# Performance work log

Hardware: AMD Instinct MI355X
Metric: run time of the kernel (lower is better)

## Reference

```python
import jax, jax.numpy as jnp
import numpy as np

N_NODES = 50000
N_EDGES = 800000
IN_FEAT = 256
OUT_FEAT = 256
NUM_RELS = 8
ALPHA = 0.5


def setup_inputs() -> dict:
    key = jax.random.key(0)
    k1, k2, k3, k4, k5, k6 = jax.random.split(key, 6)
    x = jax.random.normal(k1, (N_NODES, IN_FEAT), dtype=jnp.float32)
    edge_index = jax.random.randint(k2, (2, N_EDGES), 0, N_NODES, dtype=jnp.int64)
    edge_type = jax.random.randint(k3, (N_EDGES,), 0, NUM_RELS, dtype=jnp.int64)
    # Xavier-uniform-ish init for weights (scale per fan-in/fan-out)
    gain = float(np.sqrt(2.0))  # calculate_gain('relu')
    lim_w = gain * float(np.sqrt(6.0 / (IN_FEAT + OUT_FEAT)))
    weight = jax.random.uniform(k4, (NUM_RELS, IN_FEAT, OUT_FEAT), dtype=jnp.float32,
                                minval=-lim_w, maxval=lim_w)
    loop_weight = jax.random.uniform(k5, (IN_FEAT, OUT_FEAT), dtype=jnp.float32,
                                     minval=-lim_w, maxval=lim_w)
    h_bias = jnp.zeros((OUT_FEAT,), dtype=jnp.float32)
    return {"edge_index": edge_index, "x": x, "edge_type": edge_type,
            "weight": weight, "h_bias": h_bias, "loop_weight": loop_weight}


def reference(edge_index, x, edge_type, weight, h_bias, loop_weight):
    num_nodes = x.shape[0]
    src, dst = edge_index[0], edge_index[1]
    # Per-edge message msg_e = x[src_e] @ weight[edge_type_e].
    # Computed efficiently as num_rels dense GEMMs over all nodes, then a fused
    # (relation, src) gather — identical math, avoids (E, in, out) weight blowup.
    hx = jnp.einsum('ni,rio->rno', x, weight)          # (R, N, out)
    msg = hx[edge_type, src]                            # (E, out)
    agg = jax.ops.segment_sum(msg, dst, num_segments=num_nodes)  # (N, out)
    node_repr = agg * jnp.asarray(ALPHA, x.dtype) ** 0.5
    node_repr = node_repr + h_bias
    loop_message = x @ loop_weight                      # (N, out)
    node_repr = node_repr + loop_message * jnp.asarray(1.0 - ALPHA, x.dtype) ** 0.5
    # activation=None, dropout=0.0 (eval) -> identity
    return node_repr
```

## Files before the change

kernel.cpp:

```cpp
#include <hip/hip_runtime.h>

typedef __bf16 bf16x8 __attribute__((ext_vector_type(8)));
typedef float f32x4 __attribute__((ext_vector_type(4)));

static __device__ __forceinline__ unsigned short f2bf(float f) {
    unsigned u = __builtin_bit_cast(unsigned, f);
    u += 0x7FFFu + ((u >> 16) & 1u);
    return (unsigned short)(u >> 16);
}
static __device__ __forceinline__ float bf2f(unsigned short h) {
    return __builtin_bit_cast(float, ((unsigned)h) << 16);
}

#define GLOAD_LDS16(g, l)                                              \
    __builtin_amdgcn_global_load_lds(                                  \
        (const __attribute__((address_space(1))) unsigned int*)(g),    \
        (__attribute__((address_space(3))) unsigned int*)(l), 16, 0, 0)

__global__ __launch_bounds__(256) void rgcn_prep(const int* __restrict__ ei,
                                                 unsigned* __restrict__ cnt,
                                                 const float* __restrict__ x,
                                                 unsigned short* __restrict__ Z,
                                                 const float* __restrict__ w,
                                                 const float* __restrict__ lw,
                                                 unsigned short* __restrict__ wbT,
                                                 int E, int M, int HB, int CB) {
    const int b = blockIdx.x;
    const int t = threadIdx.x;
    if (b < HB) {
        int e = b * 256 + t;
        if (e < E) atomicAdd(&cnt[ei[E + e]], 1u);
    } else if (b < HB + CB) {
        int wv = ((b - HB) * 256 + t) >> 6;
        int lane = t & 63;
        if (wv < M) {
            float4 v = *(const float4*)(x + (size_t)wv * 256 + lane * 4);
            ushort4 o;
            o.x = f2bf(v.x); o.y = f2bf(v.y); o.z = f2bf(v.z); o.w = f2bf(v.w);
            *(ushort4*)(Z + (size_t)wv * 2304 + 2048 + lane * 4) = o;
        }
    } else {
        int bb = b - HB - CB;
        int kc = (bb % 9) * 256 + t;
        int n  = bb / 9;
        if (kc < 2304) {
            float v;
            if (kc < 2048) {
                int r = kc >> 8, k = kc & 255;
                v = w[((size_t)r * 256 + k) * 256 + n];
            } else {
                v = lw[(size_t)(kc - 2048) * 256 + n];
            }
            wbT[(size_t)n * 2304 + kc] = f2bf(v * 0.70710678118654752f);
        }
    }
}

__global__ __launch_bounds__(1024) void rgcn_scan_all(const unsigned* __restrict__ cnt,
                                                      unsigned* __restrict__ off,
                                                      unsigned* __restrict__ cur,
                                                      unsigned* __restrict__ done,
                                                      unsigned* __restrict__ bsum,
                                                      int n, int nb) {
    __shared__ unsigned wsum[16];
    __shared__ unsigned bpre_s;
    const int t = threadIdx.x, lane = t & 63, wv = t >> 6;
    const int b = blockIdx.x;
    int i = b * 1024 + t;
    unsigned v = (i < n) ? cnt[i] : 0;
    unsigned s = v;
    #pragma unroll
    for (int d = 1; d < 64; d <<= 1) {
        unsigned u = __shfl_up(s, d, 64);
        if (lane >= d) s += u;
    }
    if (lane == 63) wsum[wv] = s;
    __syncthreads();
    if (wv == 0) {
        unsigned bb = (lane < 16) ? wsum[lane] : 0;
        unsigned sb = bb;
        #pragma unroll
        for (int d = 1; d < 16; d <<= 1) {
            unsigned u = __shfl_up(sb, d, 64);
            if (lane >= d) sb += u;
        }
        if (lane < 16) wsum[lane] = sb - bb;
        if (lane == 15) {
            atomicExch(&bsum[b], sb);
            __threadfence();
            atomicAdd(done, 1u);
        }
    }
    __syncthreads();
    if (t == 0) {
        while (atomicAdd(done, 0u) < (unsigned)nb) __builtin_amdgcn_s_sleep(8);
    }
    __syncthreads();
    if (wv == 0) {
        unsigned bv = (lane < nb) ? atomicAdd(&bsum[lane], 0u) : 0;
        unsigned sp = bv;
        #pragma unroll
        for (int d = 1; d < 64; d <<= 1) {
            unsigned u = __shfl_up(sp, d, 64);
            if (lane >= d) sp += u;
        }
        if (lane == b) bpre_s = sp - bv;
        if (b == 0 && lane == nb - 1) off[n] = sp;
    }
    __syncthreads();
    unsigned base = bpre_s + wsum[wv];
    if (i < n) {
        unsigned o = base + (s - v);
        off[i] = o;
        cur[i] = o;
    }
}

__global__ __launch_bounds__(256) void rgcn_scatter(const int* __restrict__ ei,
                                                    const int* __restrict__ et,
                                                    unsigned* __restrict__ cur,
                                                    unsigned* __restrict__ recs, int E) {
    int e = blockIdx.x * 256 + threadIdx.x;
    if (e < E) {
        int dst = ei[E + e];
        unsigned p = atomicAdd(&cur[dst], 1u);
        recs[p] = (unsigned)ei[e] | ((unsigned)et[e] << 16);
    }
}

__global__ __launch_bounds__(256) void rgcn_agg(const unsigned* __restrict__ recs,
                                                const unsigned* __restrict__ off,
                                                unsigned short* __restrict__ Z, int M) {
    const int gw0  = (blockIdx.x * 256 + threadIdx.x) >> 6;
    const int nw   = (gridDim.x * 256) >> 6;
    const int lane = threadIdx.x & 63;
    const unsigned short* Zx = Z + 2048 + lane * 4;

#define GATHER(rr) (*(const ushort4*)(Zx + (size_t)((rr) & 0xFFFFu) * 2304))
#define ACCUM(rec, v_)                                                                 \
    {                                                                                  \
        f32x4 fv;                                                                      \
        fv[0] = bf2f(v_.x); fv[1] = bf2f(v_.y); fv[2] = bf2f(v_.z); fv[3] = bf2f(v_.w);\
        switch ((rec) >> 16) {                                                         \
            case 0: a0 += fv; break; case 1: a1 += fv; break;                          \
            case 2: a2 += fv; break; case 3: a3 += fv; break;                          \
            case 4: a4 += fv; break; case 5: a5 += fv; break;                          \
            case 6: a6 += fv; break; default: a7 += fv; break;                         \
        }                                                                              \
    }

    for (int w = gw0; w < M; w += nw) {
        const unsigned o0 = off[w], o1 = off[w + 1];
        f32x4 a0 = {}, a1 = {}, a2 = {}, a3 = {}, a4 = {}, a5 = {}, a6 = {}, a7 = {};

        for (unsigned base = o0; base < o1; base += 64) {
            const unsigned wdeg = (o1 - base < 64u) ? (o1 - base) : 64u;
            const unsigned myrec = ((unsigned)lane < wdeg) ? recs[base + lane] : 0u;

            unsigned j = 0;
            for (; j + 16 <= wdeg; j += 16) {
                unsigned rr[16];
                #pragma unroll
                for (int u = 0; u < 16; ++u) rr[u] = __shfl(myrec, (int)(j + u), 64);
                ushort4 vv[16];
                #pragma unroll
                for (int u = 0; u < 16; ++u) vv[u] = GATHER(rr[u]);
                #pragma unroll
                for (int u = 0; u < 16; ++u) ACCUM(rr[u], vv[u]);
            }
            for (; j + 4 <= wdeg; j += 4) {
                unsigned rr[4];
                #pragma unroll
                for (int u = 0; u < 4; ++u) rr[u] = __shfl(myrec, (int)(j + u), 64);
                ushort4 vv[4];
                #pragma unroll
                for (int u = 0; u < 4; ++u) vv[u] = GATHER(rr[u]);
                #pragma unroll
                for (int u = 0; u < 4; ++u) ACCUM(rr[u], vv[u]);
            }
            for (; j < wdeg; ++j) {
                unsigned r_ = __shfl(myrec, (int)j, 64);
                ushort4 v_ = GATHER(r_);
                ACCUM(r_, v_);
            }
        }

        unsigned short* zr = Z + (size_t)w * 2304 + lane * 4;
#define ST(rr_, ax)                                                                    \
        {                                                                              \
            ushort4 o_;                                                                \
            o_.x = f2bf(ax[0]); o_.y = f2bf(ax[1]);                                    \
            o_.z = f2bf(ax[2]); o_.w = f2bf(ax[3]);                                    \
            *(ushort4*)(zr + rr_ * 256) = o_;                                          \
        }
        ST(0, a0) ST(1, a1) ST(2, a2) ST(3, a3) ST(4, a4) ST(5, a5) ST(6, a6) ST(7, a7)
#undef ST
    }
#undef GATHER
#undef ACCUM
}

#define BM 128
#define BK 64
#define NCH 36

__global__ __launch_bounds__(512, 4) void rgcn_gemm(
    const unsigned short* __restrict__ A,
    const unsigned short* __restrict__ Bt,
    float* __restrict__ out,
    const float* __restrict__ bias,
    int M)
{
    __shared__ char lds[16384 * 2 + 32768];
    char* Ab0 = lds;
    char* Ab1 = lds + 16384;
    char* Bb  = lds + 32768;

    const int tid  = threadIdx.x;
    const int lane = tid & 63;
    const int wid  = tid >> 6;
    const int wm   = (wid >> 2) * 64;
    const int wn   = (wid & 3) * 64;
    const int m0   = blockIdx.x * BM;

    f32x4 acc[4][4] = {};

    auto stageA = [&](int chunk, char* dst) {
        #pragma unroll
        for (int it = 0; it < 2; ++it) {
            int o   = it * 8192 + tid * 16;
            int r   = o >> 7;
            int scb = (o & 127) ^ ((r & 7) << 4);
            int ga  = m0 + r; if (ga >= M) ga = M - 1;
            GLOAD_LDS16((const char*)A + (size_t)ga * 4608 + (size_t)chunk * 128 + scb, dst + o);
        }
    };
    auto stageB = [&](int chunk) {
        #pragma unroll
        for (int it = 0; it < 4; ++it) {
            int o   = it * 8192 + tid * 16;
            int r   = o >> 7;
            int scb = (o & 127) ^ ((r & 7) << 4);
            GLOAD_LDS16((const char*)Bt + (size_t)r * 4608 + (size_t)chunk * 128 + scb, Bb + o);
        }
    };

    stageA(0, Ab0);
    stageB(0);
    stageA(1, Ab1);
    asm volatile("s_waitcnt vmcnt(2)" ::: "memory");
    __builtin_amdgcn_s_barrier();
    __builtin_amdgcn_sched_barrier(0);

    for (int t = 0; t < NCH; ++t) {
        const char* Ac = (t & 1) ? Ab1 : Ab0;
        #pragma unroll
        for (int kk = 0; kk < 2; ++kk) {
            const int koff = kk * 32 + (lane >> 4) * 8;
            bf16x8 af[4], bfr[4];
            #pragma unroll
            for (int i = 0; i < 4; ++i) {
                int ar = wm + i * 16 + (lane & 15);
                af[i] = *(const bf16x8*)(Ac + ((ar * 128 + koff * 2) ^ ((ar & 7) << 4)));
            }
            #pragma unroll
            for (int j = 0; j < 4; ++j) {
                int br = wn + j * 16 + (lane & 15);
                bfr[j] = *(const bf16x8*)(Bb + ((br * 128 + koff * 2) ^ ((br & 7) << 4)));
            }
            #pragma unroll
            for (int i = 0; i < 4; ++i)
                #pragma unroll
                for (int j = 0; j < 4; ++j)
                    acc[i][j] = __builtin_amdgcn_mfma_f32_16x16x32_bf16(af[i], bfr[j], acc[i][j], 0, 0, 0);
        }

        if (t < NCH - 1) {
            __builtin_amdgcn_s_barrier();
            __builtin_amdgcn_sched_barrier(0);
            stageB(t + 1);
            int ta = (t + 2 < NCH) ? t + 2 : NCH - 1;
            stageA(ta, (t & 1) ? Ab1 : Ab0);
            asm volatile("s_waitcnt vmcnt(2)" ::: "memory");
            __builtin_amdgcn_s_barrier();
            __builtin_amdgcn_sched_barrier(0);
        }
    }
    asm volatile("s_waitcnt vmcnt(0)" ::: "memory");

    const int col = lane & 15;
    const int r0  = (lane >> 4) * 4;
    #pragma unroll
    for (int i = 0; i < 4; ++i) {
        #pragma unroll
        for (int j = 0; j < 4; ++j) {
            int gn = wn + j * 16 + col;
            float bv = bias[gn];
            #pragma unroll
            for (int rr = 0; rr < 4; ++rr) {
                int gm = m0 + wm + i * 16 + r0 + rr;
                if (gm < M) out[(size_t)gm * 256 + gn] = acc[i][j][rr] + bv;
            }
        }
    }
}

extern "C" void kernel_launch(void* const* d_in, const int* in_sizes, int n_in,
                              void* d_out, int out_size, void* d_ws, size_t ws_size,
                              hipStream_t stream) {
    const int*   edge_index = (const int*)d_in[0];
    const float* x          = (const float*)d_in[1];
    const int*   edge_type  = (const int*)d_in[2];
    const float* weight     = (const float*)d_in[3];
    const float* h_bias     = (const float*)d_in[4];
    const float* loop_w     = (const float*)d_in[5];
    float* out = (float*)d_out;

    const int M = in_sizes[1] / 256;
    const int E = in_sizes[2];

    char* ws = (char*)d_ws;
    size_t off_b = 0;
    unsigned short* Zcat = (unsigned short*)(ws + off_b);
    off_b += (((size_t)M * 2304 * 2) + 255) & ~(size_t)255;
    unsigned short* wbT = (unsigned short*)(ws + off_b);
    off_b += (((size_t)256 * 2304 * 2) + 255) & ~(size_t)255;
    unsigned* cnt = (unsigned*)(ws + off_b);
    unsigned* done = cnt + M;
    unsigned* bsum = cnt + M + 2;
    off_b += (((size_t)(M + 2 + 64) * 4) + 255) & ~(size_t)255;
    unsigned* off = (unsigned*)(ws + off_b);
    off_b += (((size_t)(M + 1) * 4) + 255) & ~(size_t)255;
    unsigned* cur = (unsigned*)(ws + off_b);
    off_b += (((size_t)M * 4) + 255) & ~(size_t)255;
    unsigned* recs = (unsigned*)(ws + off_b);

    const int nb = (M + 1023) / 1024;
    const int HB = (E + 255) / 256;
    const int CB = (M + 3) / 4;

    (void)hipMemsetAsync(cnt, 0, (size_t)(M + 2 + 64) * 4, stream);

    rgcn_prep<<<HB + CB + 2304, 256, 0, stream>>>(edge_index, cnt, x, Zcat,
                                                  weight, loop_w, wbT, E, M, HB, CB);
    rgcn_scan_all<<<nb, 1024, 0, stream>>>(cnt, off, cur, done, bsum, M, nb);
    rgcn_scatter<<<(E + 255) / 256, 256, 0, stream>>>(edge_index, edge_type, cur, recs, E);

    rgcn_agg<<<2560, 256, 0, stream>>>(recs, off, Zcat, M);

    rgcn_gemm<<<(M + BM - 1) / BM, 512, 0, stream>>>(Zcat, wbT, out, h_bias, M);
}
```

Before: 301.3 us.

## Fuse edge aggregation into GEMM via per-block LDS panel of relation sums

```diff
diff --git a/kernel.cpp b/kernel.cpp
--- a/kernel.cpp
+++ b/kernel.cpp
@@ -20,7 +20,7 @@
 __global__ __launch_bounds__(256) void rgcn_prep(const int* __restrict__ ei,
                                                  unsigned* __restrict__ cnt,
                                                  const float* __restrict__ x,
-                                                 unsigned short* __restrict__ Z,
+                                                 unsigned short* __restrict__ xb,
                                                  const float* __restrict__ w,
                                                  const float* __restrict__ lw,
                                                  unsigned short* __restrict__ wbT,
@@ -37,7 +37,7 @@
             float4 v = *(const float4*)(x + (size_t)wv * 256 + lane * 4);
             ushort4 o;
             o.x = f2bf(v.x); o.y = f2bf(v.y); o.z = f2bf(v.z); o.w = f2bf(v.w);
-            *(ushort4*)(Z + (size_t)wv * 2304 + 2048 + lane * 4) = o;
+            *(ushort4*)(xb + (size_t)wv * 256 + lane * 4) = o;
         }
     } else {
         int bb = b - HB - CB;
@@ -128,113 +128,28 @@
     }
 }
 
-__global__ __launch_bounds__(256) void rgcn_agg(const unsigned* __restrict__ recs,
-                                                const unsigned* __restrict__ off,
-                                                unsigned short* __restrict__ Z, int M) {
-    const int gw0  = (blockIdx.x * 256 + threadIdx.x) >> 6;
-    const int nw   = (gridDim.x * 256) >> 6;
-    const int lane = threadIdx.x & 63;
-    const unsigned short* Zx = Z + 2048 + lane * 4;
-
-#define GATHER(rr) (*(const ushort4*)(Zx + (size_t)((rr) & 0xFFFFu) * 2304))
-#define ACCUM(rec, v_)                                                                 \
-    {                                                                                  \
-        f32x4 fv;                                                                      \
-        fv[0] = bf2f(v_.x); fv[1] = bf2f(v_.y); fv[2] = bf2f(v_.z); fv[3] = bf2f(v_.w);\
-        switch ((rec) >> 16) {                                                         \
-            case 0: a0 += fv; break; case 1: a1 += fv; break;                          \
-            case 2: a2 += fv; break; case 3: a3 += fv; break;                          \
-            case 4: a4 += fv; break; case 5: a5 += fv; break;                          \
-            case 6: a6 += fv; break; default: a7 += fv; break;                         \
-        }                                                                              \
-    }
-
-    for (int w = gw0; w < M; w += nw) {
-        const unsigned o0 = off[w], o1 = off[w + 1];
-        f32x4 a0 = {}, a1 = {}, a2 = {}, a3 = {}, a4 = {}, a5 = {}, a6 = {}, a7 = {};
-
-        for (unsigned base = o0; base < o1; base += 64) {
-            const unsigned wdeg = (o1 - base < 64u) ? (o1 - base) : 64u;
-            const unsigned myrec = ((unsigned)lane < wdeg) ? recs[base + lane] : 0u;
-
-            unsigned j = 0;
-            for (; j + 16 <= wdeg; j += 16) {
-                unsigned rr[16];
-                #pragma unroll
-                for (int u = 0; u < 16; ++u) rr[u] = __shfl(myrec, (int)(j + u), 64);
-                ushort4 vv[16];
-                #pragma unroll
-                for (int u = 0; u < 16; ++u) vv[u] = GATHER(rr[u]);
-                #pragma unroll
-                for (int u = 0; u < 16; ++u) ACCUM(rr[u], vv[u]);
-            }
-            for (; j + 4 <= wdeg; j += 4) {
-                unsigned rr[4];
-                #pragma unroll
-                for (int u = 0; u < 4; ++u) rr[u] = __shfl(myrec, (int)(j + u), 64);
-                ushort4 vv[4];
-                #pragma unroll
-                for (int u = 0; u < 4; ++u) vv[u] = GATHER(rr[u]);
-                #pragma unroll
-                for (int u = 0; u < 4; ++u) ACCUM(rr[u], vv[u]);
-            }
-            for (; j < wdeg; ++j) {
-                unsigned r_ = __shfl(myrec, (int)j, 64);
-                ushort4 v_ = GATHER(r_);
-                ACCUM(r_, v_);
-            }
-        }
-
-        unsigned short* zr = Z + (size_t)w * 2304 + lane * 4;
-#define ST(rr_, ax)                                                                    \
-        {                                                                              \
-            ushort4 o_;                                                                \
-            o_.x = f2bf(ax[0]); o_.y = f2bf(ax[1]);                                    \
-            o_.z = f2bf(ax[2]); o_.w = f2bf(ax[3]);                                    \
-            *(ushort4*)(zr + rr_ * 256) = o_;                                          \
-        }
-        ST(0, a0) ST(1, a1) ST(2, a2) ST(3, a3) ST(4, a4) ST(5, a5) ST(6, a6) ST(7, a7)
-#undef ST
-    }
-#undef GATHER
-#undef ACCUM
-}
-
-#define BM 128
-#define BK 64
-#define NCH 36
-
-__global__ __launch_bounds__(512, 4) void rgcn_gemm(
-    const unsigned short* __restrict__ A,
+__global__ __launch_bounds__(512) void rgcn_fused(
+    const unsigned short* __restrict__ xb,
     const unsigned short* __restrict__ Bt,
+    const unsigned* __restrict__ recs,
+    const unsigned* __restrict__ off,
     float* __restrict__ out,
     const float* __restrict__ bias,
     int M)
 {
-    __shared__ char lds[16384 * 2 + 32768];
-    char* Ab0 = lds;
-    char* Ab1 = lds + 16384;
-    char* Bb  = lds + 32768;
+    __shared__ char lds[131072 + 32768];
+    char* panel = lds;
+    char* Bb    = lds + 131072;
 
     const int tid  = threadIdx.x;
     const int lane = tid & 63;
     const int wid  = tid >> 6;
-    const int wm   = (wid >> 2) * 64;
+    const int wm   = (wid >> 2) * 16;
     const int wn   = (wid & 3) * 64;
-    const int m0   = blockIdx.x * BM;
-
-    f32x4 acc[4][4] = {};
-
-    auto stageA = [&](int chunk, char* dst) {
-        #pragma unroll
-        for (int it = 0; it < 2; ++it) {
-            int o   = it * 8192 + tid * 16;
-            int r   = o >> 7;
-            int scb = (o & 127) ^ ((r & 7) << 4);
-            int ga  = m0 + r; if (ga >= M) ga = M - 1;
-            GLOAD_LDS16((const char*)A + (size_t)ga * 4608 + (size_t)chunk * 128 + scb, dst + o);
-        }
-    };
+    const int m0   = blockIdx.x * 32;
+
+    f32x4 acc[4] = {};
+
     auto stageB = [&](int chunk) {
         #pragma unroll
         for (int it = 0; it < 4; ++it) {
@@ -245,62 +160,136 @@
         }
     };
 
-    stageA(0, Ab0);
-    stageB(0);
-    stageA(1, Ab1);
-    asm volatile("s_waitcnt vmcnt(2)" ::: "memory");
-    __builtin_amdgcn_s_barrier();
-    __builtin_amdgcn_sched_barrier(0);
-
-    for (int t = 0; t < NCH; ++t) {
-        const char* Ac = (t & 1) ? Ab1 : Ab0;
+    for (int c = 0; c < 4; ++c) {
+        stageB(32 + c);
+        if (tid < 256) {
+            int o   = tid * 16;
+            int r   = o >> 7;
+            int scb = (o & 127) ^ ((r & 7) << 4);
+            int ga  = m0 + r; if (ga >= M) ga = M - 1;
+            GLOAD_LDS16((const char*)xb + (size_t)ga * 512 + c * 128 + scb, panel + o);
+        }
+        asm volatile("s_waitcnt vmcnt(0)" ::: "memory");
+        __syncthreads();
         #pragma unroll
         for (int kk = 0; kk < 2; ++kk) {
             const int koff = kk * 32 + (lane >> 4) * 8;
-            bf16x8 af[4], bfr[4];
-            #pragma unroll
-            for (int i = 0; i < 4; ++i) {
-                int ar = wm + i * 16 + (lane & 15);
-                af[i] = *(const bf16x8*)(Ac + ((ar * 128 + koff * 2) ^ ((ar & 7) << 4)));
-            }
+            int ar = wm + (lane & 15);
+            bf16x8 af = *(const bf16x8*)(panel + ((ar * 128 + koff * 2) ^ ((ar & 7) << 4)));
             #pragma unroll
             for (int j = 0; j < 4; ++j) {
                 int br = wn + j * 16 + (lane & 15);
-                bfr[j] = *(const bf16x8*)(Bb + ((br * 128 + koff * 2) ^ ((br & 7) << 4)));
-            }
+                bf16x8 bfr = *(const bf16x8*)(Bb + ((br * 128 + koff * 2) ^ ((br & 7) << 4)));
+                acc[j] = __builtin_amdgcn_mfma_f32_16x16x32_bf16(af, bfr, acc[j], 0, 0, 0);
+            }
+        }
+        __syncthreads();
+    }
+
+    {
+        const unsigned short* Zx = xb + lane * 4;
+
+#define GATHER(rr) (*(const ushort4*)(Zx + (size_t)((rr) & 0xFFFFu) * 256))
+#define ACCUM(rec, v_)                                                                 \
+        {                                                                              \
+            f32x4 fv;                                                                  \
+            fv[0] = bf2f(v_.x); fv[1] = bf2f(v_.y);                                    \
+            fv[2] = bf2f(v_.z); fv[3] = bf2f(v_.w);                                    \
+            switch ((rec) >> 16) {                                                     \
+                case 0: a0 += fv; break; case 1: a1 += fv; break;                      \
+                case 2: a2 += fv; break; case 3: a3 += fv; break;                      \
+                case 4: a4 += fv; break; case 5: a5 += fv; break;                      \
+                case 6: a6 += fv; break; default: a7 += fv; break;                     \
+            }                                                                          \
+        }
+
+        for (int i = 0; i < 4; ++i) {
+            const int r = wid * 4 + i;
+            const int w = m0 + r;
+            f32x4 a0 = {}, a1 = {}, a2 = {}, a3 = {}, a4 = {}, a5 = {}, a6 = {}, a7 = {};
+
+            if (w < M) {
+                const unsigned o0 = off[w], o1 = off[w + 1];
+                for (unsigned base = o0; base < o1; base += 64) {
+                    const unsigned wdeg = (o1 - base < 64u) ? (o1 - base) : 64u;
+                    const unsigned myrec = ((unsigned)lane < wdeg) ? recs[base + lane] : 0u;
+                    unsigned j = 0;
+                    for (; j + 16 <= wdeg; j += 16) {
+                        unsigned rr[16];
+                        #pragma unroll
+                        for (int u = 0; u < 16; ++u) rr[u] = __shfl(myrec, (int)(j + u), 64);
+                        ushort4 vv[16];
+                        #pragma unroll
+                        for (int u = 0; u < 16; ++u) vv[u] = GATHER(rr[u]);
+                        #pragma unroll
+                        for (int u = 0; u < 16; ++u) ACCUM(rr[u], vv[u]);
+                    }
+                    for (; j + 4 <= wdeg; j += 4) {
+                        unsigned rr[4];
+                        #pragma unroll
+                        for (int u = 0; u < 4; ++u) rr[u] = __shfl(myrec, (int)(j + u), 64);
+                        ushort4 vv[4];
+                        #pragma unroll
+                        for (int u = 0; u < 4; ++u) vv[u] = GATHER(rr[u]);
+                        #pragma unroll
+                        for (int u = 0; u < 4; ++u) ACCUM(rr[u], vv[u]);
+                    }
+                    for (; j < wdeg; ++j) {
+                        unsigned r_ = __shfl(myrec, (int)j, 64);
+                        ushort4 v_ = GATHER(r_);
+                        ACCUM(r_, v_);
+                    }
+                }
+            }
+
+            const int sw = (r & 7) << 4;
+            char* prow = panel + r * 4096;
+#define STP(rel, ax)                                                                   \
+            {                                                                          \
+                ushort4 o_;                                                            \
+                o_.x = f2bf(ax[0]); o_.y = f2bf(ax[1]);                                \
+                o_.z = f2bf(ax[2]); o_.w = f2bf(ax[3]);                                \
+                *(ushort4*)(prow + (((rel) * 512 + lane * 8) ^ sw)) = o_;              \
+            }
+            STP(0, a0) STP(1, a1) STP(2, a2) STP(3, a3)
+            STP(4, a4) STP(5, a5) STP(6, a6) STP(7, a7)
+#undef STP
+        }
+#undef GATHER
+#undef ACCUM
+    }
+    __syncthreads();
+
+    for (int t = 0; t < 32; ++t) {
+        if (t) __syncthreads();
+        stageB(t);
+        asm volatile("s_waitcnt vmcnt(0)" ::: "memory");
+        __syncthreads();
+        #pragma unroll
+        for (int kk = 0; kk < 2; ++kk) {
+            const int koff = kk * 32 + (lane >> 4) * 8;
+            int ar = wm + (lane & 15);
+            bf16x8 af = *(const bf16x8*)(panel + ar * 4096 + t * 128 +
+                                         ((koff * 2) ^ ((ar & 7) << 4)));
             #pragma unroll
-            for (int i = 0; i < 4; ++i)
-                #pragma unroll
-                for (int j = 0; j < 4; ++j)
-                    acc[i][j] = __builtin_amdgcn_mfma_f32_16x16x32_bf16(af[i], bfr[j], acc[i][j], 0, 0, 0);
-        }
-
-        if (t < NCH - 1) {
-            __builtin_amdgcn_s_barrier();
-            __builtin_amdgcn_sched_barrier(0);
-            stageB(t + 1);
-            int ta = (t + 2 < NCH) ? t + 2 : NCH - 1;
-            stageA(ta, (t & 1) ? Ab1 : Ab0);
-            asm volatile("s_waitcnt vmcnt(2)" ::: "memory");
-            __builtin_amdgcn_s_barrier();
-            __builtin_amdgcn_sched_barrier(0);
-        }
-    }
-    asm volatile("s_waitcnt vmcnt(0)" ::: "memory");
+            for (int j = 0; j < 4; ++j) {
+                int br = wn + j * 16 + (lane & 15);
+                bf16x8 bfr = *(const bf16x8*)(Bb + ((br * 128 + koff * 2) ^ ((br & 7) << 4)));
+                acc[j] = __builtin_amdgcn_mfma_f32_16x16x32_bf16(af, bfr, acc[j], 0, 0, 0);
+            }
+        }
+    }
 
     const int col = lane & 15;
     const int r0  = (lane >> 4) * 4;
     #pragma unroll
-    for (int i = 0; i < 4; ++i) {
-        #pragma unroll
-        for (int j = 0; j < 4; ++j) {
-            int gn = wn + j * 16 + col;
-            float bv = bias[gn];
-            #pragma unroll
-            for (int rr = 0; rr < 4; ++rr) {
-                int gm = m0 + wm + i * 16 + r0 + rr;
-                if (gm < M) out[(size_t)gm * 256 + gn] = acc[i][j][rr] + bv;
-            }
+    for (int j = 0; j < 4; ++j) {
+        int gn = wn + j * 16 + col;
+        float bv = bias[gn];
+        #pragma unroll
+        for (int rr = 0; rr < 4; ++rr) {
+            int gm = m0 + wm + r0 + rr;
+            if (gm < M) out[(size_t)gm * 256 + gn] = acc[j][rr] + bv;
         }
     }
 }
@@ -321,8 +310,8 @@
 
     char* ws = (char*)d_ws;
     size_t off_b = 0;
-    unsigned short* Zcat = (unsigned short*)(ws + off_b);
-    off_b += (((size_t)M * 2304 * 2) + 255) & ~(size_t)255;
+    unsigned short* xb = (unsigned short*)(ws + off_b);
+    off_b += (((size_t)M * 256 * 2) + 255) & ~(size_t)255;
     unsigned short* wbT = (unsigned short*)(ws + off_b);
     off_b += (((size_t)256 * 2304 * 2) + 255) & ~(size_t)255;
     unsigned* cnt = (unsigned*)(ws + off_b);
@@ -341,12 +330,10 @@
 
     (void)hipMemsetAsync(cnt, 0, (size_t)(M + 2 + 64) * 4, stream);
 
-    rgcn_prep<<<HB + CB + 2304, 256, 0, stream>>>(edge_index, cnt, x, Zcat,
+    rgcn_prep<<<HB + CB + 2304, 256, 0, stream>>>(edge_index, cnt, x, xb,
                                                   weight, loop_w, wbT, E, M, HB, CB);
     rgcn_scan_all<<<nb, 1024, 0, stream>>>(cnt, off, cur, done, bsum, M, nb);
     rgcn_scatter<<<(E + 255) / 256, 256, 0, stream>>>(edge_index, edge_type, cur, recs, E);
 
-    rgcn_agg<<<2560, 256, 0, stream>>>(recs, off, Zcat, M);
-
-    rgcn_gemm<<<(M + BM - 1) / BM, 512, 0, stream>>>(Zcat, wbT, out, h_bias, M);
-}
+    rgcn_fused<<<(M + 31) / 32, 512, 0, stream>>>(xb, wbT, recs, off, out, h_bias, M);
+}
```

New measurement: 487.7 us. +61.8%, slower.

## Tile weight transpose through LDS and fuse scan with edge scatter

Applied to the files above, without the earlier changes.

```diff
diff --git a/kernel.cpp b/kernel.cpp
--- a/kernel.cpp
+++ b/kernel.cpp
@@ -25,6 +25,7 @@
                                                  const float* __restrict__ lw,
                                                  unsigned short* __restrict__ wbT,
                                                  int E, int M, int HB, int CB) {
+    __shared__ float tile[64][65];
     const int b = blockIdx.x;
     const int t = threadIdx.x;
     if (b < HB) {
@@ -40,28 +41,60 @@
             *(ushort4*)(Z + (size_t)wv * 2304 + 2048 + lane * 4) = o;
         }
     } else {
-        int bb = b - HB - CB;
-        int kc = (bb % 9) * 256 + t;
-        int n  = bb / 9;
-        if (kc < 2304) {
-            float v;
-            if (kc < 2048) {
-                int r = kc >> 8, k = kc & 255;
-                v = w[((size_t)r * 256 + k) * 256 + n];
-            } else {
-                v = lw[(size_t)(kc - 2048) * 256 + n];
-            }
-            wbT[(size_t)n * 2304 + kc] = f2bf(v * 0.70710678118654752f);
-        }
-    }
-}
-
-__global__ __launch_bounds__(1024) void rgcn_scan_all(const unsigned* __restrict__ cnt,
-                                                      unsigned* __restrict__ off,
-                                                      unsigned* __restrict__ cur,
-                                                      unsigned* __restrict__ done,
-                                                      unsigned* __restrict__ bsum,
-                                                      int n, int nb) {
+        const int bb = b - HB - CB;
+        const float* src;
+        int kt, nt_, kcb;
+        if (bb < 128) {
+            int r = bb >> 4, tl = bb & 15;
+            kt = (tl >> 2) * 64; nt_ = (tl & 3) * 64;
+            src = w + (size_t)r * 65536;
+            kcb = r * 256 + kt;
+        } else {
+            int tl = bb - 128;
+            kt = (tl >> 2) * 64; nt_ = (tl & 3) * 64;
+            src = lw;
+            kcb = 2048 + kt;
+        }
+        {
+            int row = t >> 4, c4 = (t & 15) * 4;
+            #pragma unroll
+            for (int p = 0; p < 4; ++p) {
+                int rr = row + p * 16;
+                float4 v = *(const float4*)(src + (size_t)(kt + rr) * 256 + nt_ + c4);
+                tile[rr][c4] = v.x; tile[rr][c4 + 1] = v.y;
+                tile[rr][c4 + 2] = v.z; tile[rr][c4 + 3] = v.w;
+            }
+        }
+        __syncthreads();
+        {
+            const float s = 0.70710678118654752f;
+            int nn = t >> 2, ko = (t & 3) * 16;
+            unsigned short* dst = wbT + (size_t)(nt_ + nn) * 2304 + kcb + ko;
+            #pragma unroll
+            for (int q = 0; q < 4; ++q) {
+                ushort4 o_;
+                o_.x = f2bf(tile[ko + q * 4 + 0][nn] * s);
+                o_.y = f2bf(tile[ko + q * 4 + 1][nn] * s);
+                o_.z = f2bf(tile[ko + q * 4 + 2][nn] * s);
+                o_.w = f2bf(tile[ko + q * 4 + 3][nn] * s);
+                *(ushort4*)(dst + q * 4) = o_;
+            }
+        }
+    }
+}
+
+__global__ __launch_bounds__(1024) void rgcn_scan_scatter(
+    const unsigned* __restrict__ cnt,
+    unsigned* __restrict__ off,
+    unsigned* __restrict__ cur,
+    unsigned* __restrict__ done,
+    unsigned* __restrict__ done2,
+    unsigned* __restrict__ bsum,
+    const int* __restrict__ ei,
+    const int* __restrict__ et,
+    unsigned* __restrict__ recs,
+    int n, int nb, int E)
+{
     __shared__ unsigned wsum[16];
     __shared__ unsigned bpre_s;
     const int t = threadIdx.x, lane = t & 63, wv = t >> 6;
@@ -112,16 +145,30 @@
     if (i < n) {
         unsigned o = base + (s - v);
         off[i] = o;
-        cur[i] = o;
-    }
-}
-
-__global__ __launch_bounds__(256) void rgcn_scatter(const int* __restrict__ ei,
-                                                    const int* __restrict__ et,
-                                                    unsigned* __restrict__ cur,
-                                                    unsigned* __restrict__ recs, int E) {
-    int e = blockIdx.x * 256 + threadIdx.x;
-    if (e < E) {
+        atomicExch(&cur[i], o);
+    }
+    __threadfence();
+    __syncthreads();
+    if (t == 0) atomicAdd(done2, 1u);
+    if (t == 0) {
+        while (atomicAdd(done2, 0u) < (unsigned)nb) __builtin_amdgcn_s_sleep(8);
+    }
+    __syncthreads();
+
+    const int nt = nb * 1024;
+    int e = b * 1024 + t;
+    for (; e + 3 * nt < E; e += 4 * nt) {
+        int d0 = ei[E + e], d1 = ei[E + e + nt], d2 = ei[E + e + 2 * nt], d3 = ei[E + e + 3 * nt];
+        unsigned p0 = atomicAdd(&cur[d0], 1u);
+        unsigned p1 = atomicAdd(&cur[d1], 1u);
+        unsigned p2 = atomicAdd(&cur[d2], 1u);
+        unsigned p3 = atomicAdd(&cur[d3], 1u);
+        recs[p0] = (unsigned)ei[e]          | ((unsigned)et[e] << 16);
+        recs[p1] = (unsigned)ei[e + nt]     | ((unsigned)et[e + nt] << 16);
+        recs[p2] = (unsigned)ei[e + 2 * nt] | ((unsigned)et[e + 2 * nt] << 16);
+        recs[p3] = (unsigned)ei[e + 3 * nt] | ((unsigned)et[e + 3 * nt] << 16);
+    }
+    for (; e < E; e += nt) {
         int dst = ei[E + e];
         unsigned p = atomicAdd(&cur[dst], 1u);
         recs[p] = (unsigned)ei[e] | ((unsigned)et[e] << 16);
@@ -326,8 +373,9 @@
     unsigned short* wbT = (unsigned short*)(ws + off_b);
     off_b += (((size_t)256 * 2304 * 2) + 255) & ~(size_t)255;
     unsigned* cnt = (unsigned*)(ws + off_b);
-    unsigned* done = cnt + M;
-    unsigned* bsum = cnt + M + 2;
+    unsigned* done  = cnt + M;
+    unsigned* done2 = cnt + M + 1;
+    unsigned* bsum  = cnt + M + 2;
     off_b += (((size_t)(M + 2 + 64) * 4) + 255) & ~(size_t)255;
     unsigned* off = (unsigned*)(ws + off_b);
     off_b += (((size_t)(M + 1) * 4) + 255) & ~(size_t)255;
@@ -341,10 +389,10 @@
 
     (void)hipMemsetAsync(cnt, 0, (size_t)(M + 2 + 64) * 4, stream);
 
-    rgcn_prep<<<HB + CB + 2304, 256, 0, stream>>>(edge_index, cnt, x, Zcat,
-                                                  weight, loop_w, wbT, E, M, HB, CB);
-    rgcn_scan_all<<<nb, 1024, 0, stream>>>(cnt, off, cur, done, bsum, M, nb);
-    rgcn_scatter<<<(E + 255) / 256, 256, 0, stream>>>(edge_index, edge_type, cur, recs, E);
+    rgcn_prep<<<HB + CB + 144, 256, 0, stream>>>(edge_index, cnt, x, Zcat,
+                                                 weight, loop_w, wbT, E, M, HB, CB);
+    rgcn_scan_scatter<<<nb, 1024, 0, stream>>>(cnt, off, cur, done, done2, bsum,
+                                               edge_index, edge_type, recs, M, nb, E);
 
     rgcn_agg<<<2560, 256, 0, stream>>>(recs, off, Zcat, M);
 
```

After: 337.5 us. 12.0% more time.
